# Kernel optimization log

Hardware: AMD Instinct MI355X
Metric: run time of the kernel (lower is better)

## Reference

```python
import jax, jax.numpy as jnp
import numpy as np

B, C, L, K, R = 32, 64, 16384, 3, 8

def _lrelu(x):
    return jnp.where(x >= 0, x, 0.1 * x)

def setup_inputs() -> dict:
    key = jax.random.key(0)
    ks = jax.random.split(key, 8)
    s = lambda i, shape: (jax.random.normal(ks[i], shape, jnp.float32) * 0.05)
    return {
        "x0": jax.random.normal(ks[0], (B, C, L), jnp.float32),
        "x1": jax.random.normal(ks[1], (B, 64), jnp.float32),
        "W1": s(2, (64, 64)),           # Linear(64,64).weight [out,in]
        "W2": s(3, (64 * K, 64)),       # Linear(64,64*K).weight
        "conv_w": s(4, (C, C)),         # 1x1 Conv1d weight [out,in]
        "conv_b": s(5, (C,)),
        "ca_w1": s(6, (C // R, C)),     # CA conv1 weight
        "ca_w2": s(7, (C, C // R)),     # CA conv2 weight
    }

def reference(x0, x1, W1, W2, conv_w, conv_b, ca_w1, ca_w2):
    b, c, l = x0.shape
    k = W2.shape[0] // 64
    pad = (k - 1) // 2
    # dynamic per-(b,c) depthwise kernels
    h = _lrelu(x1 @ W1.T)                         # [b,64]
    kern = (h @ W2.T).reshape(b, c, k)            # [b,c,k]
    # depthwise conv1d (cross-correlation), groups=b*c
    xp = jnp.pad(x0, ((0, 0), (0, 0), (pad, pad)))
    out = sum(xp[:, :, j:j + l] * kern[:, :, j:j + 1] for j in range(k))
    out = _lrelu(out)
    # 1x1 conv
    out = jnp.einsum('bcl,oc->bol', out, conv_w) + conv_b[None, :, None]
    # channel attention gate on x1
    att = jax.nn.sigmoid(_lrelu(x1 @ ca_w1.T) @ ca_w2.T)  # [b,c]
    return out + x0 * att[:, :, None]
```

## Files before the change

kernel.cpp:

```cpp
#include <hip/hip_runtime.h>
#include <math.h>

#define B_ 32
#define C_ 64
#define L_ 16384
#define LT 128

typedef __attribute__((ext_vector_type(8))) short short8;
typedef __attribute__((ext_vector_type(4))) float f32x4;

__device__ __forceinline__ unsigned short f2bf(float x) {
  unsigned int u = __builtin_bit_cast(unsigned int, x);
  u += 0x7fffu + ((u >> 16) & 1u);
  return (unsigned short)(u >> 16);
}

__device__ __forceinline__ float lrelu(float x) {
  return x >= 0.f ? x : 0.1f * x;
}

__device__ __forceinline__ void load_lds_16(const void* g, void* l) {
  __builtin_amdgcn_global_load_lds(
      (const __attribute__((address_space(1))) void*)g,
      (__attribute__((address_space(3))) void*)l, 16, 0, 0);
}

__global__ void da_prep(const float* __restrict__ x1,
                        const float* __restrict__ W1,
                        const float* __restrict__ W2,
                        const float* __restrict__ ca_w1,
                        const float* __restrict__ ca_w2,
                        float* __restrict__ kern,
                        float* __restrict__ att) {
  int b = blockIdx.x;
  int t = threadIdx.x;
  __shared__ float x1s[64], h[64], a1[8];
  x1s[t] = x1[b * 64 + t];
  __syncthreads();
  {
    const float* w1r = W1 + t * 64;
    float s = 0.f;
    #pragma unroll
    for (int i = 0; i < 64; ++i) s = fmaf(x1s[i], w1r[i], s);
    h[t] = lrelu(s);
  }
  if (t < 8) {
    const float* cw = ca_w1 + t * 64;
    float a = 0.f;
    #pragma unroll
    for (int i = 0; i < 64; ++i) a = fmaf(x1s[i], cw[i], a);
    a1[t] = lrelu(a);
  }
  __syncthreads();
  #pragma unroll
  for (int kk = 0; kk < 3; ++kk) {
    const float* w2r = W2 + (t * 3 + kk) * 64;
    float s2 = 0.f;
    #pragma unroll
    for (int i = 0; i < 64; ++i) s2 = fmaf(h[i], w2r[i], s2);
    kern[(b * 64 + t) * 3 + kk] = s2;
  }
  {
    float a = 0.f;
    #pragma unroll
    for (int r = 0; r < 8; ++r) a = fmaf(a1[r], ca_w2[t * 8 + r], a);
    att[b * 64 + t] = 1.f / (1.f + expf(-a));
  }
}

__global__ __launch_bounds__(256) void da_main(
    const float* __restrict__ x0,
    const float* __restrict__ conv_w,
    const float* __restrict__ conv_b,
    const float* __restrict__ kern,
    const float* __restrict__ att,
    float* __restrict__ out) {
  __shared__ float x0s[64 * LT];
  __shared__ unsigned short midT[LT * 64];
  __shared__ float cbs[64], atts[64];

  int blk = blockIdx.x;
  int b = blk >> 7;
  int l0 = (blk & 127) * LT;
  int tid = threadIdx.x;
  int lane = tid & 63;
  int wave = tid >> 6;

  int m_lane = lane & 15;
  int kbase = (lane >> 4) * 8;

  {
    int p = lane & 31;
    int rsel = lane >> 5;
    #pragma unroll
    for (int i = 0; i < 8; ++i) {
      int c = wave * 16 + i * 2 + rsel;
      const float* g = x0 + ((size_t)(b * 64 + c)) * L_ + l0 + ((p ^ (c & 7)) << 2);
      load_lds_16(g, &x0s[(wave * 16 + i * 2) * LT]);
    }
  }

  if (tid < 64) {
    cbs[tid] = conv_b[tid];
    atts[tid] = att[b * 64 + tid];
  }
  float k0, k1, k2;
  {
    const float* kr = kern + (b * 64 + lane) * 3;
    k0 = kr[0]; k1 = kr[1]; k2 = kr[2];
  }
  float prev_g = 0.f, nxt_g = 0.f;
  {
    const float* xrow = x0 + ((size_t)(b * 64 + lane)) * L_;
    if (wave == 0 && l0 > 0) prev_g = xrow[l0 - 1];
    if (wave == 3 && l0 + LT < L_) nxt_g = xrow[l0 + LT];
  }

  short8 af[2][4];
  #pragma unroll
  for (int kt = 0; kt < 2; ++kt) {
    #pragma unroll
    for (int mt = 0; mt < 4; ++mt) {
      const float* wr = conv_w + (mt * 16 + m_lane) * 64 + kt * 32 + kbase;
      float4 wa = *(const float4*)wr;
      float4 wb = *(const float4*)(wr + 4);
      short8 v;
      v[0] = (short)f2bf(wa.x); v[1] = (short)f2bf(wa.y);
      v[2] = (short)f2bf(wa.z); v[3] = (short)f2bf(wa.w);
      v[4] = (short)f2bf(wb.x); v[5] = (short)f2bf(wb.y);
      v[6] = (short)f2bf(wb.z); v[7] = (short)f2bf(wb.w);
      af[kt][mt] = v;
    }
  }

  asm volatile("s_waitcnt vmcnt(0)" ::: "memory");
  __syncthreads();

  {
    int c = lane;
    int w0 = wave * 32;
    const int rowb = c * LT;
    const int csw = (c & 7) << 2;

    float4 q[8];
    #pragma unroll
    for (int i = 0; i < 8; ++i) {
      int chunk = (w0 >> 2) + i;
      q[i] = *(const float4*)&x0s[rowb + ((chunk << 2) ^ csw)];
    }
    float prev, nxt;
    if (wave == 0) {
      prev = prev_g;
    } else {
      int w = w0 - 1;
      prev = x0s[rowb + ((w & ~3) ^ csw) + (w & 3)];
    }
    if (wave == 3) {
      nxt = nxt_g;
    } else {
      int w = w0 + 32;
      nxt = x0s[rowb + ((w & ~3) ^ csw) + (w & 3)];
    }

    #pragma unroll
    for (int i = 0; i < 8; ++i) {
      float xa = q[i].x, xb = q[i].y, xc = q[i].z, xd = q[i].w;
      float xm1 = prev;
      if (i > 0) xm1 = q[i - 1].w;
      float xp1 = nxt;
      if (i < 7) xp1 = q[i + 1].x;
      float m0 = fmaf(k0, xm1, fmaf(k1, xa, k2 * xb));
      float m1 = fmaf(k0, xa,  fmaf(k1, xb, k2 * xc));
      float m2 = fmaf(k0, xb,  fmaf(k1, xc, k2 * xd));
      float m3 = fmaf(k0, xc,  fmaf(k1, xd, k2 * xp1));
      int l = w0 + 4 * i;
      midT[(l + 0) * 64 + (c ^ (((l + 0) & 7) << 3))] = f2bf(lrelu(m0));
      midT[(l + 1) * 64 + (c ^ (((l + 1) & 7) << 3))] = f2bf(lrelu(m1));
      midT[(l + 2) * 64 + (c ^ (((l + 2) & 7) << 3))] = f2bf(lrelu(m2));
      midT[(l + 3) * 64 + (c ^ (((l + 3) & 7) << 3))] = f2bf(lrelu(m3));
    }
  }
  __syncthreads();

  f32x4 acc[4][2];
  #pragma unroll
  for (int mt = 0; mt < 4; ++mt)
    #pragma unroll
    for (int nt = 0; nt < 2; ++nt)
      acc[mt][nt] = (f32x4){0.f, 0.f, 0.f, 0.f};

  int lw = wave * 32;
  #pragma unroll
  for (int kt = 0; kt < 2; ++kt) {
    #pragma unroll
    for (int nt = 0; nt < 2; ++nt) {
      int l = lw + nt * 16 + m_lane;
      int cb = kt * 32 + kbase;
      const short8 bf = *(const short8*)&midT[l * 64 + (cb ^ ((l & 7) << 3))];
      #pragma unroll
      for (int mt = 0; mt < 4; ++mt)
        acc[mt][nt] = __builtin_amdgcn_mfma_f32_16x16x32_bf16(
            af[kt][mt], bf, acc[mt][nt], 0, 0, 0);
    }
  }

  int r0 = (lane >> 4) * 4;
  int ln = lane & 15;
  #pragma unroll
  for (int mt = 0; mt < 4; ++mt) {
    #pragma unroll
    for (int r = 0; r < 4; ++r) {
      int o = mt * 16 + r0 + r;
      float bias = cbs[o];
      float a = atts[o];
      const int orow = o * LT;
      const int osw = (o & 7) << 2;
      float* outr = out + ((size_t)(b * 64 + o)) * L_ + l0;
      #pragma unroll
      for (int nt = 0; nt < 2; ++nt) {
        int l = lw + nt * 16 + ln;
        float xv = x0s[orow + ((l & ~3) ^ osw) + (l & 3)];
        outr[l] = acc[mt][nt][r] + bias + xv * a;
      }
    }
  }
}

extern "C" void kernel_launch(void* const* d_in, const int* in_sizes, int n_in,
                              void* d_out, int out_size, void* d_ws, size_t ws_size,
                              hipStream_t stream) {
  const float* x0     = (const float*)d_in[0];
  const float* x1     = (const float*)d_in[1];
  const float* W1     = (const float*)d_in[2];
  const float* W2     = (const float*)d_in[3];
  const float* conv_w = (const float*)d_in[4];
  const float* conv_b = (const float*)d_in[5];
  const float* ca_w1  = (const float*)d_in[6];
  const float* ca_w2  = (const float*)d_in[7];
  float* out = (float*)d_out;

  float* kern = (float*)d_ws;
  float* att  = kern + B_ * C_ * 3;

  da_prep<<<dim3(B_), dim3(64), 0, stream>>>(x1, W1, W2, ca_w1, ca_w2, kern, att);
  da_main<<<dim3(B_ * (L_ / LT)), dim3(256), 0, stream>>>(x0, conv_w, conv_b,
                                                          kern, att, out);
}
```

Before: 76.61 us.

## Make da_main persistent over 8 L-tiles with double-buffered async x0 loads

```diff
diff --git a/kernel.cpp b/kernel.cpp
--- a/kernel.cpp
+++ b/kernel.cpp
@@ -4,7 +4,9 @@
 #define B_ 32
 #define C_ 64
 #define L_ 16384
-#define LT 128
+#define LT 64
+#define NT 8
+#define NBLK (B_ * (L_ / LT / NT))
 
 typedef __attribute__((ext_vector_type(8))) short short8;
 typedef __attribute__((ext_vector_type(4))) float f32x4;
@@ -68,20 +70,20 @@
   }
 }
 
-__global__ __launch_bounds__(256) void da_main(
+__global__ __launch_bounds__(256, 3) void da_main(
     const float* __restrict__ x0,
     const float* __restrict__ conv_w,
     const float* __restrict__ conv_b,
     const float* __restrict__ kern,
     const float* __restrict__ att,
     float* __restrict__ out) {
-  __shared__ float x0s[64 * LT];
+  __shared__ float x0s[2][64 * LT];
   __shared__ unsigned short midT[LT * 64];
   __shared__ float cbs[64], atts[64];
 
-  int blk = blockIdx.x;
-  int b = blk >> 7;
-  int l0 = (blk & 127) * LT;
+  int bid = blockIdx.x;
+  int b = bid >> 5;
+  int base_l = (bid & 31) * (NT * LT);
   int tid = threadIdx.x;
   int lane = tid & 63;
   int wave = tid >> 6;
@@ -89,15 +91,26 @@
   int m_lane = lane & 15;
   int kbase = (lane >> 4) * 8;
 
-  {
-    int p = lane & 31;
-    int rsel = lane >> 5;
-    #pragma unroll
-    for (int i = 0; i < 8; ++i) {
-      int c = wave * 16 + i * 2 + rsel;
-      const float* g = x0 + ((size_t)(b * 64 + c)) * L_ + l0 + ((p ^ (c & 7)) << 2);
-      load_lds_16(g, &x0s[(wave * 16 + i * 2) * LT]);
-    }
+  const float* xb = x0 + (size_t)(b * 64) * L_;
+
+  auto STAGE = [&](int t0, int d) {
+    int l0t = base_l + t0 * LT;
+    int p = lane & 15;
+    int r4 = lane >> 4;
+    #pragma unroll
+    for (int i = 0; i < 4; ++i) {
+      int c = wave * 16 + i * 4 + r4;
+      const float* g = xb + (size_t)c * L_ + l0t + ((p ^ (c & 7)) << 2);
+      load_lds_16(g, &x0s[d][(wave * 16 + i * 4) * LT]);
+    }
+  };
+
+  STAGE(0, 0);
+  float hp[2] = {0.f, 0.f}, hn[2] = {0.f, 0.f};
+  {
+    int l0t = base_l;
+    if (wave == 0 && l0t > 0) hp[0] = xb[(size_t)lane * L_ + l0t - 1];
+    if (wave == 3 && l0t + LT < L_) hn[0] = xb[(size_t)lane * L_ + l0t + LT];
   }
 
   if (tid < 64) {
@@ -109,13 +122,6 @@
     const float* kr = kern + (b * 64 + lane) * 3;
     k0 = kr[0]; k1 = kr[1]; k2 = kr[2];
   }
-  float prev_g = 0.f, nxt_g = 0.f;
-  {
-    const float* xrow = x0 + ((size_t)(b * 64 + lane)) * L_;
-    if (wave == 0 && l0 > 0) prev_g = xrow[l0 - 1];
-    if (wave == 3 && l0 + LT < L_) nxt_g = xrow[l0 + LT];
-  }
-
   short8 af[2][4];
   #pragma unroll
   for (int kt = 0; kt < 2; ++kt) {
@@ -133,95 +139,100 @@
     }
   }
 
-  asm volatile("s_waitcnt vmcnt(0)" ::: "memory");
-  __syncthreads();
-
-  {
-    int c = lane;
-    int w0 = wave * 32;
-    const int rowb = c * LT;
-    const int csw = (c & 7) << 2;
-
-    float4 q[8];
-    #pragma unroll
-    for (int i = 0; i < 8; ++i) {
-      int chunk = (w0 >> 2) + i;
-      q[i] = *(const float4*)&x0s[rowb + ((chunk << 2) ^ csw)];
-    }
-    float prev, nxt;
-    if (wave == 0) {
-      prev = prev_g;
-    } else {
-      int w = w0 - 1;
-      prev = x0s[rowb + ((w & ~3) ^ csw) + (w & 3)];
-    }
-    if (wave == 3) {
-      nxt = nxt_g;
-    } else {
-      int w = w0 + 32;
-      nxt = x0s[rowb + ((w & ~3) ^ csw) + (w & 3)];
-    }
-
-    #pragma unroll
-    for (int i = 0; i < 8; ++i) {
-      float xa = q[i].x, xb = q[i].y, xc = q[i].z, xd = q[i].w;
-      float xm1 = prev;
-      if (i > 0) xm1 = q[i - 1].w;
-      float xp1 = nxt;
-      if (i < 7) xp1 = q[i + 1].x;
-      float m0 = fmaf(k0, xm1, fmaf(k1, xa, k2 * xb));
-      float m1 = fmaf(k0, xa,  fmaf(k1, xb, k2 * xc));
-      float m2 = fmaf(k0, xb,  fmaf(k1, xc, k2 * xd));
-      float m3 = fmaf(k0, xc,  fmaf(k1, xd, k2 * xp1));
-      int l = w0 + 4 * i;
-      midT[(l + 0) * 64 + (c ^ (((l + 0) & 7) << 3))] = f2bf(lrelu(m0));
-      midT[(l + 1) * 64 + (c ^ (((l + 1) & 7) << 3))] = f2bf(lrelu(m1));
-      midT[(l + 2) * 64 + (c ^ (((l + 2) & 7) << 3))] = f2bf(lrelu(m2));
-      midT[(l + 3) * 64 + (c ^ (((l + 3) & 7) << 3))] = f2bf(lrelu(m3));
-    }
-  }
-  __syncthreads();
-
-  f32x4 acc[4][2];
   #pragma unroll
-  for (int mt = 0; mt < 4; ++mt)
-    #pragma unroll
-    for (int nt = 0; nt < 2; ++nt)
-      acc[mt][nt] = (f32x4){0.f, 0.f, 0.f, 0.f};
-
-  int lw = wave * 32;
-  #pragma unroll
-  for (int kt = 0; kt < 2; ++kt) {
-    #pragma unroll
-    for (int nt = 0; nt < 2; ++nt) {
-      int l = lw + nt * 16 + m_lane;
+  for (int t = 0; t < NT; ++t) {
+    const int d = t & 1;
+
+    if (t + 1 < NT) {
+      STAGE(t + 1, d ^ 1);
+      int l0n = base_l + (t + 1) * LT;
+      if (wave == 0) hp[(t + 1) & 1] = xb[(size_t)lane * L_ + l0n - 1];
+      if (wave == 3)
+        hn[(t + 1) & 1] = (l0n + LT < L_) ? xb[(size_t)lane * L_ + l0n + LT] : 0.f;
+    }
+
+    if (t == 0)
+      asm volatile("s_waitcnt vmcnt(4) lgkmcnt(0)" ::: "memory");
+    else if (t == NT - 1)
+      asm volatile("s_waitcnt vmcnt(16) lgkmcnt(0)" ::: "memory");
+    else
+      asm volatile("s_waitcnt vmcnt(20) lgkmcnt(0)" ::: "memory");
+    __builtin_amdgcn_s_barrier();
+
+    {
+      int c = lane;
+      int w0 = wave * 16;
+      const float* row = &x0s[d][c * LT];
+      const int csw = (c & 7) << 2;
+
+      float4 q[4];
+      #pragma unroll
+      for (int i = 0; i < 4; ++i)
+        q[i] = *(const float4*)&row[((wave * 4 + i) ^ (c & 7)) << 2];
+
+      float prev = (wave == 0)
+          ? hp[t & 1]
+          : row[(((w0 - 1) & ~3) ^ csw) + ((w0 - 1) & 3)];
+      float nxt = (wave == 3)
+          ? hn[t & 1]
+          : row[(((w0 + 16) & ~3) ^ csw) + ((w0 + 16) & 3)];
+
+      #pragma unroll
+      for (int i = 0; i < 4; ++i) {
+        float xa = q[i].x, xb2 = q[i].y, xc = q[i].z, xd = q[i].w;
+        float xm1 = prev;
+        if (i > 0) xm1 = q[i - 1].w;
+        float xp1 = nxt;
+        if (i < 3) xp1 = q[i + 1].x;
+        float m0 = fmaf(k0, xm1, fmaf(k1, xa,  k2 * xb2));
+        float m1 = fmaf(k0, xa,  fmaf(k1, xb2, k2 * xc));
+        float m2 = fmaf(k0, xb2, fmaf(k1, xc,  k2 * xd));
+        float m3 = fmaf(k0, xc,  fmaf(k1, xd,  k2 * xp1));
+        int l = w0 + 4 * i;
+        midT[(l + 0) * 64 + (c ^ (((l + 0) & 7) << 3))] = f2bf(lrelu(m0));
+        midT[(l + 1) * 64 + (c ^ (((l + 1) & 7) << 3))] = f2bf(lrelu(m1));
+        midT[(l + 2) * 64 + (c ^ (((l + 2) & 7) << 3))] = f2bf(lrelu(m2));
+        midT[(l + 3) * 64 + (c ^ (((l + 3) & 7) << 3))] = f2bf(lrelu(m3));
+      }
+    }
+
+    asm volatile("s_waitcnt lgkmcnt(0)" ::: "memory");
+    __builtin_amdgcn_s_barrier();
+
+    f32x4 acc[4];
+    #pragma unroll
+    for (int mt = 0; mt < 4; ++mt) acc[mt] = (f32x4){0.f, 0.f, 0.f, 0.f};
+    int lw = wave * 16;
+    #pragma unroll
+    for (int kt = 0; kt < 2; ++kt) {
+      int l = lw + m_lane;
       int cb = kt * 32 + kbase;
       const short8 bf = *(const short8*)&midT[l * 64 + (cb ^ ((l & 7) << 3))];
       #pragma unroll
       for (int mt = 0; mt < 4; ++mt)
-        acc[mt][nt] = __builtin_amdgcn_mfma_f32_16x16x32_bf16(
-            af[kt][mt], bf, acc[mt][nt], 0, 0, 0);
-    }
-  }
-
-  int r0 = (lane >> 4) * 4;
-  int ln = lane & 15;
-  #pragma unroll
-  for (int mt = 0; mt < 4; ++mt) {
-    #pragma unroll
-    for (int r = 0; r < 4; ++r) {
-      int o = mt * 16 + r0 + r;
-      float bias = cbs[o];
-      float a = atts[o];
-      const int orow = o * LT;
-      const int osw = (o & 7) << 2;
-      float* outr = out + ((size_t)(b * 64 + o)) * L_ + l0;
-      #pragma unroll
-      for (int nt = 0; nt < 2; ++nt) {
-        int l = lw + nt * 16 + ln;
-        float xv = x0s[orow + ((l & ~3) ^ osw) + (l & 3)];
-        outr[l] = acc[mt][nt][r] + bias + xv * a;
+        acc[mt] = __builtin_amdgcn_mfma_f32_16x16x32_bf16(af[kt][mt], bf,
+                                                          acc[mt], 0, 0, 0);
+    }
+
+    {
+      int l0t = base_l + t * LT;
+      int r0 = (lane >> 4) * 4;
+      int w = lw + m_lane;
+      #pragma unroll
+      for (int mt = 0; mt < 4; ++mt) {
+        #pragma unroll
+        for (int r = 0; r < 4; ++r) {
+          int o = mt * 16 + r0 + r;
+          float xv = x0s[d][o * LT + (((w & ~3) ^ ((o & 7) << 2)) + (w & 3))];
+          out[(size_t)(b * 64 + o) * L_ + l0t + w] =
+              acc[mt][r] + cbs[o] + xv * atts[o];
+        }
       }
+    }
+
+    if (t + 1 < NT) {
+      asm volatile("s_waitcnt lgkmcnt(0)" ::: "memory");
+      __builtin_amdgcn_s_barrier();
     }
   }
 }
@@ -243,6 +254,6 @@
   float* att  = kern + B_ * C_ * 3;
 
   da_prep<<<dim3(B_), dim3(64), 0, stream>>>(x1, W1, W2, ca_w1, ca_w2, kern, att);
-  da_main<<<dim3(B_ * (L_ / LT)), dim3(256), 0, stream>>>(x0, conv_w, conv_b,
-                                                          kern, att, out);
-}
+  da_main<<<dim3(NBLK), dim3(256), 0, stream>>>(x0, conv_w, conv_b,
+                                                kern, att, out);
+}
```

After: 79.69 us. 1.04x slower.
